# Kernel tuning notes

Hardware: AMD Instinct MI355X
Metric: run time of the kernel (lower is better)

## Reference

```python
import jax, jax.numpy as jnp
import numpy as np

N_LAST = 4096  # power of two; K=1 path of get_hadK


def fwht(x):
    """Fast Walsh-Hadamard transform along the last dim, normalized by 1/sqrt(n).
    Matches QuaRot matmul_hadU butterfly recursion (K=1, power-of-two n)."""
    n = x.shape[-1]
    y = x.reshape(-1, n, 1)  # (B, n, 1)
    while y.shape[1] > 1:
        y = y.reshape(y.shape[0], y.shape[1] // 2, 2, y.shape[2])
        a = y[:, :, 0, :]
        b = y[:, :, 1, :]
        # butterfly: interleave (a+b, a-b) back into the trailing dim
        y = jnp.concatenate([a + b, a - b], axis=-1)  # (B, m/2, 2k)
    return y.reshape(x.shape) * np.float32(1.0 / np.sqrt(n))


def setup_inputs() -> dict:
    key = jax.random.key(0)
    x = jax.random.normal(key, (4, 2048, N_LAST), dtype=jnp.float32)
    return {"x": x}


def reference(x) -> jnp.ndarray:
    # HadamardTransform.forward with do_rotate=True
    dtype = x.dtype
    return fwht(x).astype(dtype)
```

## Files before the change

kernel.cpp:

```cpp
#include <hip/hip_runtime.h>


constexpr int N = 4096;
constexpr int PAD = 65;

__device__ __forceinline__ void wht64(float v[64]) {
#pragma unroll
    for (int m = 1; m < 64; m <<= 1) {
#pragma unroll
        for (int g = 0; g < 64; g += 2 * m) {
#pragma unroll
            for (int k = 0; k < m; ++k) {
                float a = v[g + k];
                float b = v[g + k + m];
                v[g + k]     = a + b;
                v[g + k + m] = a - b;
            }
        }
    }
}

__global__ __launch_bounds__(64, 2) void fwht4096_kernel(const float* __restrict__ in,
                                                         float* __restrict__ out) {
    __shared__ float lds[64 * PAD];

    const int l = threadIdx.x;
    const size_t row = blockIdx.x;
    const float* __restrict__ src = in + row * (size_t)N;
    float* __restrict__ dst = out + row * (size_t)N;

    float v[64];

#pragma unroll
    for (int j = 0; j < 64; ++j) v[j] = src[j * 64 + l];

    wht64(v);

    {
        const int wbase = l;
#pragma unroll
        for (int j = 0; j < 64; ++j) lds[wbase + j * PAD] = v[j];
    }
    __syncthreads();
    {
        const int rbase = l * PAD;
#pragma unroll
        for (int k = 0; k < 64; ++k) v[k] = lds[rbase + k];
    }

    wht64(v);

    const float scale = 0.015625f;
    float4* __restrict__ d4 = (float4*)(dst + l * 64);
#pragma unroll
    for (int r = 0; r < 16; ++r) {
        d4[r] = make_float4(v[4 * r + 0] * scale, v[4 * r + 1] * scale,
                            v[4 * r + 2] * scale, v[4 * r + 3] * scale);
    }
}

extern "C" void kernel_launch(void* const* d_in, const int* in_sizes, int n_in,
                              void* d_out, int out_size, void* d_ws, size_t ws_size,
                              hipStream_t stream) {
    const float* x = (const float*)d_in[0];
    float* y = (float*)d_out;
    const int rows = in_sizes[0] / N;
    fwht4096_kernel<<<rows, 64, 0, stream>>>(x, y);
}
```

Measured before the change: 250.6 us.

## Restructure FWHT into three radix-16 LDS passes with direct global-to-LDS loads

Replaces the two radix-64 register passes with three radix-16 passes staged through LDS. The input is loaded straight into LDS with global_load_lds, 16-byte at a time, and the output is written with coalesced float4 stores. XOR swizzles and sign fixups keep LDS access bank-friendly. The aim is to cut register pressure from 64-float arrays and to get coalesced, wide global access, at the cost of more LDS traffic and intricate index math. Barriers are replaced by waitcnt only, which is safe only because the block is a single wavefront.

```diff
diff --git a/kernel.cpp b/kernel.cpp
--- a/kernel.cpp
+++ b/kernel.cpp
@@ -2,60 +2,122 @@
 
 
 constexpr int N = 4096;
-constexpr int PAD = 65;
 
-__device__ __forceinline__ void wht64(float v[64]) {
+__device__ __forceinline__ void wht16(float v[16]) {
 #pragma unroll
-    for (int m = 1; m < 64; m <<= 1) {
+    for (int m = 1; m < 16; m <<= 1)
 #pragma unroll
-        for (int g = 0; g < 64; g += 2 * m) {
+        for (int g = 0; g < 16; g += 2 * m)
 #pragma unroll
             for (int k = 0; k < m; ++k) {
-                float a = v[g + k];
-                float b = v[g + k + m];
+                float a = v[g + k], b = v[g + k + m];
                 v[g + k]     = a + b;
                 v[g + k + m] = a - b;
             }
-        }
-    }
 }
 
-__global__ __launch_bounds__(64, 2) void fwht4096_kernel(const float* __restrict__ in,
-                                                         float* __restrict__ out) {
-    __shared__ float lds[64 * PAD];
+__global__ __launch_bounds__(64) void fwht4096_kernel(const float* __restrict__ in,
+                                                      float* __restrict__ out) {
+    __shared__ __align__(16) float lds[N];
 
     const int l = threadIdx.x;
     const size_t row = blockIdx.x;
     const float* __restrict__ src = in + row * (size_t)N;
     float* __restrict__ dst = out + row * (size_t)N;
 
-    float v[64];
+    {
+        const float* gp = src + l * 4;
+#pragma unroll
+        for (int k = 0; k < 16; ++k) {
+            __builtin_amdgcn_global_load_lds(
+                (const __attribute__((address_space(1))) unsigned int*)(gp + k * 256),
+                (__attribute__((address_space(3))) unsigned int*)(lds + k * 256),
+                16, 0, 0);
+        }
+    }
+    asm volatile("s_waitcnt vmcnt(0)" ::: "memory");
+
+    float v[16];
+    const int rb = (l >> 4) & 1;
+    const int m  = l & 15;
+    const int tb = m ^ rb;
 
 #pragma unroll
-    for (int j = 0; j < 64; ++j) v[j] = src[j * 64 + l];
+    for (int q = 0; q < 4; ++q) {
+        const int g = l + 64 * q;
+#pragma unroll
+        for (int k = 0; k < 16; ++k) v[k] = lds[k * 256 + g];
+        wht16(v);
+#pragma unroll
+        for (int k = 0; k < 16; ++k) lds[k * 256 + g] = v[k];
+    }
+    asm volatile("s_waitcnt lgkmcnt(0)" ::: "memory");
 
-    wht64(v);
+#pragma unroll
+    for (int q = 0; q < 4; ++q) {
+        const int c  = (l >> 4) + 4 * q;
+        const int e0 = c * 256 + m + 16 * rb;
+        const int e1 = c * 256 + m + 16 * (1 - rb);
+#pragma unroll
+        for (int t = 0; t < 8; ++t) {
+            v[2 * t]     = lds[e0 + 32 * t];
+            v[2 * t + 1] = lds[e1 + 32 * t];
+        }
+        wht16(v);
+#pragma unroll
+        for (int t = 0; t < 8; ++t) {
+            lds[e0 + 32 * t] = v[2 * t];
+            lds[e1 + 32 * t] = v[2 * t + 1];
+        }
+    }
+    asm volatile("s_waitcnt lgkmcnt(0)" ::: "memory");
+
+#pragma unroll
+    for (int q = 0; q < 4; ++q) {
+        const int c  = (l >> 4) + 4 * q;
+        const int ra = (c + (m >> 1)) & 3;
+        const int sw = (c + (tb >> 1)) & 3;
+        const float4* lp4 = (const float4*)lds;
+        const int rbase = c * 64 + m * 4;
+        float4 ch0 = lp4[rbase + (0 ^ ra)];
+        float4 ch1 = lp4[rbase + (1 ^ ra)];
+        float4 ch2 = lp4[rbase + (2 ^ ra)];
+        float4 ch3 = lp4[rbase + (3 ^ ra)];
+        v[0]=ch0.x;  v[1]=ch0.y;  v[2]=ch0.z;  v[3]=ch0.w;
+        v[4]=ch1.x;  v[5]=ch1.y;  v[6]=ch1.z;  v[7]=ch1.w;
+        v[8]=ch2.x;  v[9]=ch2.y;  v[10]=ch2.z; v[11]=ch2.w;
+        v[12]=ch3.x; v[13]=ch3.y; v[14]=ch3.z; v[15]=ch3.w;
+        wht16(v);
+        const float bs  = (tb & rb) ? -0.015625f : 0.015625f;
+        const float gs0 = bs;
+        const float gs1 = (ra & 1) ? -bs : bs;
+        const float gs2 = (ra & 2) ? -bs : bs;
+        const float gs3 = (((ra & 1) ^ ((ra >> 1) & 1))) ? -bs : bs;
+        float4* wp4 = (float4*)lds;
+        const int wbase = c * 64 + tb * 4;
+        wp4[wbase + (0 ^ sw)] = make_float4(v[0]*gs0,  v[1]*gs0,  v[2]*gs0,  v[3]*gs0);
+        wp4[wbase + (1 ^ sw)] = make_float4(v[4]*gs1,  v[5]*gs1,  v[6]*gs1,  v[7]*gs1);
+        wp4[wbase + (2 ^ sw)] = make_float4(v[8]*gs2,  v[9]*gs2,  v[10]*gs2, v[11]*gs2);
+        wp4[wbase + (3 ^ sw)] = make_float4(v[12]*gs3, v[13]*gs3, v[14]*gs3, v[15]*gs3);
+    }
+    asm volatile("s_waitcnt lgkmcnt(0)" ::: "memory");
 
     {
-        const int wbase = l;
+        const int l3  = l >> 3;
+        const int lo  = l & 3;
+        const int rb4 = (l >> 2) * 4;
+        const int off0 = rb4 + (lo ^ ((0 + l3) & 3));
+        const int off1 = rb4 + (lo ^ ((1 + l3) & 3));
+        const int off2 = rb4 + (lo ^ ((2 + l3) & 3));
+        const int off3 = rb4 + (lo ^ ((3 + l3) & 3));
+        const float4* lp4 = (const float4*)lds;
 #pragma unroll
-        for (int j = 0; j < 64; ++j) lds[wbase + j * PAD] = v[j];
-    }
-    __syncthreads();
-    {
-        const int rbase = l * PAD;
-#pragma unroll
-        for (int k = 0; k < 64; ++k) v[k] = lds[rbase + k];
-    }
-
-    wht64(v);
-
-    const float scale = 0.015625f;
-    float4* __restrict__ d4 = (float4*)(dst + l * 64);
-#pragma unroll
-    for (int r = 0; r < 16; ++r) {
-        d4[r] = make_float4(v[4 * r + 0] * scale, v[4 * r + 1] * scale,
-                            v[4 * r + 2] * scale, v[4 * r + 3] * scale);
+        for (int k = 0; k < 16; ++k) {
+            const int kk = k & 3;
+            const int off = (kk == 0) ? off0 : (kk == 1) ? off1 : (kk == 2) ? off2 : off3;
+            float4 val = lp4[k * 64 + off];
+            *(float4*)(dst + k * 256 + 4 * l) = val;
+        }
     }
 }
 
```

Result: faster. 229.7 us (-8.3%).
